# Kernel optimization log

Measured on AMD Instinct MI355X. Metric: run time of the kernel, lower is better.

## Reference

```python
import jax, jax.numpy as jnp
import numpy as np

N = 100000
E = 1600000
IN, HID, OUT = 128, 128, 64


def _sage_conv(x, edge_index, W_l, W_r, b):
    # PyG SAGEConv (aggr='mean'): out_i = W_l @ mean_{j->i} x_j + W_r @ x_i + b
    src, dst = edge_index[0], edge_index[1]
    msg = x[src]  # [E, d] gather
    agg = jax.ops.segment_sum(msg, dst, num_segments=N)  # [N, d]
    cnt = jax.ops.segment_sum(jnp.ones((edge_index.shape[1],), x.dtype), dst, num_segments=N)
    agg = agg / jnp.maximum(cnt, 1.0)[:, None]  # mean, safe for isolated nodes
    return agg @ W_l + x @ W_r + b


def setup_inputs() -> dict:
    key = jax.random.key(0)
    ks = jax.random.split(key, 8)
    x = jax.random.normal(ks[0], (N, IN), dtype=jnp.float32)
    W1_l = jax.random.normal(ks[1], (IN, HID), dtype=jnp.float32) / np.sqrt(IN)
    W1_r = jax.random.normal(ks[2], (IN, HID), dtype=jnp.float32) / np.sqrt(IN)
    b1 = jnp.zeros((HID,), dtype=jnp.float32)
    W2_l = jax.random.normal(ks[3], (HID, OUT), dtype=jnp.float32) / np.sqrt(HID)
    W2_r = jax.random.normal(ks[4], (HID, OUT), dtype=jnp.float32) / np.sqrt(HID)
    b2 = jnp.zeros((OUT,), dtype=jnp.float32)
    edge_index1 = jax.random.randint(ks[5], (2, E), 0, N, dtype=jnp.int64)
    edge_index2 = jax.random.randint(ks[6], (2, E), 0, N, dtype=jnp.int64)
    return {"x": x, "W1_l": W1_l, "W1_r": W1_r, "b1": b1,
            "W2_l": W2_l, "W2_r": W2_r, "b2": b2,
            "edge_index1": edge_index1, "edge_index2": edge_index2}


def reference(x, W1_l, W1_r, b1, W2_l, W2_r, b2, edge_index1, edge_index2):
    h = _sage_conv(x, edge_index1, W1_l, W1_r, b1)
    h = jax.nn.relu(h)
    h = _sage_conv(h, edge_index2, W2_l, W2_r, b2)
    return jax.nn.softmax(h, axis=1)
```

## Files before the change

kernel.cpp:

```cpp
#include <hip/hip_runtime.h>


#define FEAT 128
#define OUTF 64
#define BSH 9
#define BNODES 512
#define NBMAX 256
#define BUCKET_BLOCKS 512

typedef __attribute__((ext_vector_type(8))) short bf16x8;
typedef __attribute__((ext_vector_type(4))) float f32x4;

__device__ __forceinline__ unsigned f2bf_rne(float f) {
    unsigned u = __float_as_uint(f);
    return (u + 0x7fffu + ((u >> 16) & 1u)) >> 16;
}
__device__ __forceinline__ float bf_lo(unsigned u) { return __uint_as_float(u << 16); }
__device__ __forceinline__ float bf_hi(unsigned u) { return __uint_as_float(u & 0xffff0000u); }

__global__ void detect_idx_kernel(const unsigned* __restrict__ ei, unsigned* __restrict__ flag) {
    unsigned v = ei[2 * threadIdx.x + 1];
    if (v != 0u) atomicOr(flag, 1u);
}

__global__ __launch_bounds__(256) void convert_kernel(
    const float* __restrict__ in, unsigned short* __restrict__ outb, int total4) {
    for (int i = blockIdx.x * 256 + threadIdx.x; i < total4; i += gridDim.x * 256) {
        float4 v = *(const float4*)&in[(size_t)i * 4];
        ushort4 o;
        o.x = (unsigned short)f2bf_rne(v.x);
        o.y = (unsigned short)f2bf_rne(v.y);
        o.z = (unsigned short)f2bf_rne(v.z);
        o.w = (unsigned short)f2bf_rne(v.w);
        *(ushort4*)&outb[(size_t)i * 4] = o;
    }
}

__global__ __launch_bounds__(256) void init_cnt2_kernel(
    unsigned* __restrict__ cnt1, unsigned* __restrict__ cnt2, unsigned cap, int nb) {
    int i = blockIdx.x * 256 + threadIdx.x;
    if (i < nb) { cnt1[i] = (unsigned)i * cap; cnt2[i] = (unsigned)i * cap; }
}

__global__ __launch_bounds__(256) void bucket2_kernel(
    const void* __restrict__ ei1_raw, const void* __restrict__ ei2_raw,
    unsigned* __restrict__ pairs1, unsigned* __restrict__ pairs2,
    unsigned* __restrict__ cnt1, unsigned* __restrict__ cnt2,
    const unsigned* __restrict__ flag, int e1, int e2, unsigned cap, int nb) {
    __shared__ unsigned hist[NBMAX];
    __shared__ unsigned offs[NBMAX];
    const int tid = threadIdx.x;
    const bool is32 = (*flag != 0u);
    const int side = blockIdx.x / BUCKET_BLOCKS;
    const int bid = blockIdx.x % BUCKET_BLOCKS;
    const void* ei_raw = side ? ei2_raw : ei1_raw;
    unsigned* pairs = side ? pairs2 : pairs1;
    unsigned* cnt = side ? cnt2 : cnt1;
    const int nedge = side ? e2 : e1;
    const int chunk = (nedge + BUCKET_BLOCKS - 1) / BUCKET_BLOCKS;
    const int e0 = bid * chunk;
    const int eEnd = min(e0 + chunk, nedge);
    if (e0 >= nedge) return;

    for (int i = tid; i < nb; i += 256) hist[i] = 0u;
    __syncthreads();
    for (int e = e0 + tid; e < eEnd; e += 256) {
        int dst = is32 ? ((const int*)ei_raw)[nedge + e]
                       : (int)((const long long*)ei_raw)[nedge + e];
        atomicAdd(&hist[(unsigned)dst >> BSH], 1u);
    }
    __syncthreads();
    for (int i = tid; i < nb; i += 256) {
        unsigned c = hist[i];
        offs[i] = c ? atomicAdd(&cnt[i], c) : 0u;
    }
    __syncthreads();
    for (int e = e0 + tid; e < eEnd; e += 256) {
        int src, dst;
        if (is32) {
            const int* ei = (const int*)ei_raw;
            src = ei[e]; dst = ei[nedge + e];
        } else {
            const long long* ei = (const long long*)ei_raw;
            src = (int)ei[e]; dst = (int)ei[nedge + e];
        }
        unsigned b = (unsigned)dst >> BSH;
        unsigned pos = atomicAdd(&offs[b], 1u);
        if (pos < (b + 1u) * cap)
            pairs[pos] = (((unsigned)dst & (BNODES - 1u)) << 17) | (unsigned)src;
    }
}

__global__ __launch_bounds__(256) void csr2_kernel(
    const unsigned* __restrict__ pairs1, const unsigned* __restrict__ pairs2,
    const unsigned* __restrict__ cnt1, const unsigned* __restrict__ cnt2,
    unsigned* __restrict__ rps1, unsigned* __restrict__ rpe1,
    unsigned* __restrict__ rps2, unsigned* __restrict__ rpe2,
    int* __restrict__ esrc1, int* __restrict__ esrc2,
    unsigned cap, int n, int nb) {
    __shared__ unsigned hist[BNODES], excl[BNODES], offs[BNODES];
    __shared__ unsigned wsum[4], woff[4];
    const int side = blockIdx.x / nb;
    const int b = blockIdx.x % nb;
    const unsigned* pairs = side ? pairs2 : pairs1;
    const unsigned* cnt = side ? cnt2 : cnt1;
    unsigned* rps = side ? rps2 : rps1;
    unsigned* rpe = side ? rpe2 : rpe1;
    int* esrc = side ? esrc2 : esrc1;
    const int tid = threadIdx.x;
    const int lane = tid & 63;
    const unsigned base = (unsigned)b * cap;
    unsigned count = cnt[b] - base;
    if (count > cap) count = cap;

    hist[tid] = 0u; hist[tid + 256] = 0u;
    __syncthreads();
    for (unsigned e = tid; e < count; e += 256)
        atomicAdd(&hist[pairs[base + e] >> 17], 1u);
    __syncthreads();
    {
        unsigned s0 = hist[2 * tid], s1 = hist[2 * tid + 1];
        unsigned tsum = s0 + s1;
        unsigned incl = tsum;
        #pragma unroll
        for (int off = 1; off < 64; off <<= 1) {
            unsigned t = __shfl_up(incl, off, 64);
            if (lane >= off) incl += t;
        }
        if (lane == 63) wsum[tid >> 6] = incl;
        __syncthreads();
        if (tid == 0) {
            unsigned s = 0;
            #pragma unroll
            for (int w = 0; w < 4; ++w) { unsigned t = wsum[w]; woff[w] = s; s += t; }
        }
        __syncthreads();
        unsigned pre = woff[tid >> 6] + incl - tsum;
        excl[2 * tid] = pre;
        excl[2 * tid + 1] = pre + s0;
    }
    __syncthreads();
    #pragma unroll
    for (int h = 0; h < 2; ++h) {
        int lt = tid + h * 256;
        int node = b * BNODES + lt;
        if (node < n) {
            rps[node] = base + excl[lt];
            rpe[node] = base + excl[lt] + hist[lt];
        }
        offs[lt] = excl[lt];
    }
    __syncthreads();
    for (unsigned e = tid; e < count; e += 256) {
        unsigned p = pairs[base + e];
        unsigned lpos = atomicAdd(&offs[p >> 17], 1u);
        esrc[base + lpos] = (int)(p & 0x1FFFFu);
    }
}

#define ACC8(v)                                                              \
    a0 += bf_lo((v).x); a1 += bf_hi((v).x);                                  \
    a2 += bf_lo((v).y); a3 += bf_hi((v).y);                                  \
    a4 += bf_lo((v).z); a5 += bf_hi((v).z);                                  \
    a6 += bf_lo((v).w); a7 += bf_hi((v).w);

__global__ __launch_bounds__(256) void gather_mean128_kernel(
    const uint4* __restrict__ featq, const unsigned* __restrict__ rps,
    const unsigned* __restrict__ rpe, const int* __restrict__ esrc,
    uint4* __restrict__ aggq, int n) {
    const int wave = threadIdx.x >> 6;
    const int lane = threadIdx.x & 63;
    const int qi = lane >> 4;
    const int li = lane & 15;
    for (int node = blockIdx.x * 4 + wave; node < n; node += gridDim.x * 4) {
        unsigned rs = rps[node];
        unsigned re = rpe[node];
        float a0 = 0.f, a1 = 0.f, a2 = 0.f, a3 = 0.f;
        float a4 = 0.f, a5 = 0.f, a6 = 0.f, a7 = 0.f;
        unsigned j = rs;
        for (; j + 16 <= re; j += 16) {
            int i0 = esrc[j + qi];
            int i1 = esrc[j + 4 + qi];
            int i2 = esrc[j + 8 + qi];
            int i3 = esrc[j + 12 + qi];
            uint4 v0 = featq[(size_t)i0 * 16 + li];
            uint4 v1 = featq[(size_t)i1 * 16 + li];
            uint4 v2 = featq[(size_t)i2 * 16 + li];
            uint4 v3 = featq[(size_t)i3 * 16 + li];
            ACC8(v0); ACC8(v1); ACC8(v2); ACC8(v3);
        }
        for (; j + 8 <= re; j += 8) {
            int i0 = esrc[j + qi];
            int i1 = esrc[j + 4 + qi];
            uint4 v0 = featq[(size_t)i0 * 16 + li];
            uint4 v1 = featq[(size_t)i1 * 16 + li];
            ACC8(v0); ACC8(v1);
        }
        for (; j + 4 <= re; j += 4) {
            int i0 = esrc[j + qi];
            uint4 v0 = featq[(size_t)i0 * 16 + li];
            ACC8(v0);
        }
        unsigned rem = re - j;
        if ((unsigned)qi < rem) {
            int i0 = esrc[j + qi];
            uint4 v0 = featq[(size_t)i0 * 16 + li];
            ACC8(v0);
        }
        a0 += __shfl_xor(a0, 16, 64); a1 += __shfl_xor(a1, 16, 64);
        a2 += __shfl_xor(a2, 16, 64); a3 += __shfl_xor(a3, 16, 64);
        a4 += __shfl_xor(a4, 16, 64); a5 += __shfl_xor(a5, 16, 64);
        a6 += __shfl_xor(a6, 16, 64); a7 += __shfl_xor(a7, 16, 64);
        a0 += __shfl_xor(a0, 32, 64); a1 += __shfl_xor(a1, 32, 64);
        a2 += __shfl_xor(a2, 32, 64); a3 += __shfl_xor(a3, 32, 64);
        a4 += __shfl_xor(a4, 32, 64); a5 += __shfl_xor(a5, 32, 64);
        a6 += __shfl_xor(a6, 32, 64); a7 += __shfl_xor(a7, 32, 64);
        if (lane < 16) {
            float inv = (re > rs) ? 1.0f / (float)(re - rs) : 0.0f;
            uint4 o;
            o.x = f2bf_rne(a0 * inv) | (f2bf_rne(a1 * inv) << 16);
            o.y = f2bf_rne(a2 * inv) | (f2bf_rne(a3 * inv) << 16);
            o.z = f2bf_rne(a4 * inv) | (f2bf_rne(a5 * inv) << 16);
            o.w = f2bf_rne(a6 * inv) | (f2bf_rne(a7 * inv) << 16);
            aggq[(size_t)node * 16 + lane] = o;
        }
    }
}

__global__ __launch_bounds__(256) void gather_mean64_kernel(
    const uint4* __restrict__ y2q, const unsigned* __restrict__ rps,
    const unsigned* __restrict__ rpe, const int* __restrict__ esrc,
    uint4* __restrict__ aggyq, int n) {
    const int wave = threadIdx.x >> 6;
    const int lane = threadIdx.x & 63;
    const int oi = lane >> 3;
    const int li = lane & 7;
    for (int node = blockIdx.x * 4 + wave; node < n; node += gridDim.x * 4) {
        unsigned rs = rps[node];
        unsigned re = rpe[node];
        float a0 = 0.f, a1 = 0.f, a2 = 0.f, a3 = 0.f;
        float a4 = 0.f, a5 = 0.f, a6 = 0.f, a7 = 0.f;
        unsigned j = rs;
        for (; j + 16 <= re; j += 16) {
            int i0 = esrc[j + oi];
            int i1 = esrc[j + 8 + oi];
            uint4 v0 = y2q[(size_t)i0 * 8 + li];
            uint4 v1 = y2q[(size_t)i1 * 8 + li];
            ACC8(v0); ACC8(v1);
        }
        for (; j + 8 <= re; j += 8) {
            int i0 = esrc[j + oi];
            uint4 v0 = y2q[(size_t)i0 * 8 + li];
            ACC8(v0);
        }
        unsigned rem = re - j;
        if ((unsigned)oi < rem) {
            int i0 = esrc[j + oi];
            uint4 v0 = y2q[(size_t)i0 * 8 + li];
            ACC8(v0);
        }
        a0 += __shfl_xor(a0, 8, 64);  a1 += __shfl_xor(a1, 8, 64);
        a2 += __shfl_xor(a2, 8, 64);  a3 += __shfl_xor(a3, 8, 64);
        a4 += __shfl_xor(a4, 8, 64);  a5 += __shfl_xor(a5, 8, 64);
        a6 += __shfl_xor(a6, 8, 64);  a7 += __shfl_xor(a7, 8, 64);
        a0 += __shfl_xor(a0, 16, 64); a1 += __shfl_xor(a1, 16, 64);
        a2 += __shfl_xor(a2, 16, 64); a3 += __shfl_xor(a3, 16, 64);
        a4 += __shfl_xor(a4, 16, 64); a5 += __shfl_xor(a5, 16, 64);
        a6 += __shfl_xor(a6, 16, 64); a7 += __shfl_xor(a7, 16, 64);
        a0 += __shfl_xor(a0, 32, 64); a1 += __shfl_xor(a1, 32, 64);
        a2 += __shfl_xor(a2, 32, 64); a3 += __shfl_xor(a3, 32, 64);
        a4 += __shfl_xor(a4, 32, 64); a5 += __shfl_xor(a5, 32, 64);
        a6 += __shfl_xor(a6, 32, 64); a7 += __shfl_xor(a7, 32, 64);
        if (lane < 8) {
            float inv = (re > rs) ? 1.0f / (float)(re - rs) : 0.0f;
            uint4 o;
            o.x = f2bf_rne(a0 * inv) | (f2bf_rne(a1 * inv) << 16);
            o.y = f2bf_rne(a2 * inv) | (f2bf_rne(a3 * inv) << 16);
            o.z = f2bf_rne(a4 * inv) | (f2bf_rne(a5 * inv) << 16);
            o.w = f2bf_rne(a6 * inv) | (f2bf_rne(a7 * inv) << 16);
            aggyq[(size_t)node * 8 + lane] = o;
        }
    }
}

__global__ __launch_bounds__(256, 2) void gemm1_kernel(
    const unsigned short* __restrict__ agg, const unsigned short* __restrict__ xb,
    const float* __restrict__ Wl, const float* __restrict__ Wr,
    const float* __restrict__ b, unsigned short* __restrict__ hb, int n) {
    __shared__ __align__(16) unsigned short sB[256 * FEAT];
    const int tid = threadIdx.x;

    for (int idx = tid; idx < 256 * FEAT; idx += 256) {
        int k = idx >> 7, col = idx & 127;
        float w = (k < 128) ? Wl[k * FEAT + col] : Wr[(k - 128) * FEAT + col];
        int pos = ((col >> 4) * 8 + (k >> 5)) * 512
                + ((((k >> 3) & 3) * 16 + (col & 15)) * 8) + (k & 7);
        sB[pos] = (unsigned short)f2bf_rne(w);
    }
    __syncthreads();

    const int wv = tid >> 6, lane = tid & 63;
    const int cg = wv & 1;
    const int ms = wv >> 1;
    const int g = lane >> 4, c15 = lane & 15;

    bf16x8 bf[4][8];
    #pragma unroll
    for (int ct = 0; ct < 4; ++ct)
        #pragma unroll
        for (int ks = 0; ks < 8; ++ks)
            bf[ct][ks] = *(const bf16x8*)&sB[(((cg * 4 + ct) * 8 + ks) * 64 + lane) * 8];

    float bias[4];
    #pragma unroll
    for (int ct = 0; ct < 4; ++ct) bias[ct] = b[cg * 64 + ct * 16 + c15];

    const int ntiles = (n + 31) >> 5;
    for (int tile = blockIdx.x; tile < ntiles; tile += gridDim.x) {
        const int base = tile * 32;
        const int row = base + ms * 16 + c15;
        bf16x8 af[8];
        #pragma unroll
        for (int ks = 0; ks < 8; ++ks) {
            bf16x8 a = {0, 0, 0, 0, 0, 0, 0, 0};
            if (row < n) {
                int karr = ks * 32 + g * 8;
                const unsigned short* p = (ks < 4)
                    ? &agg[(size_t)row * FEAT + karr]
                    : &xb[(size_t)row * FEAT + (karr - 128)];
                a = *(const bf16x8*)p;
            }
            af[ks] = a;
        }
        f32x4 z = {0.f, 0.f, 0.f, 0.f};
        f32x4 acc[4] = {z, z, z, z};
        #pragma unroll
        for (int ks = 0; ks < 8; ++ks)
            #pragma unroll
            for (int ct = 0; ct < 4; ++ct)
                acc[ct] = __builtin_amdgcn_mfma_f32_16x16x32_bf16(
                    af[ks], bf[ct][ks], acc[ct], 0, 0, 0);
        #pragma unroll
        for (int ct = 0; ct < 4; ++ct) {
            const int col = cg * 64 + ct * 16 + c15;
            #pragma unroll
            for (int r = 0; r < 4; ++r) {
                int node = base + ms * 16 + g * 4 + r;
                if (node < n) {
                    float v = fmaxf(acc[ct][r] + bias[ct], 0.f);
                    hb[(size_t)node * FEAT + col] = (unsigned short)f2bf_rne(v);
                }
            }
        }
    }
}

__global__ __launch_bounds__(256, 2) void gemmy2_kernel(
    const unsigned short* __restrict__ hb, const float* __restrict__ Wl,
    unsigned short* __restrict__ y2, int n) {
    __shared__ __align__(16) unsigned short sB[128 * OUTF];
    const int tid = threadIdx.x;

    for (int idx = tid; idx < 128 * OUTF; idx += 256) {
        int k = idx >> 6, col = idx & 63;
        float w = Wl[k * OUTF + col];
        int pos = ((col >> 4) * 4 + (k >> 5)) * 512
                + ((((k >> 3) & 3) * 16 + (col & 15)) * 8) + (k & 7);
        sB[pos] = (unsigned short)f2bf_rne(w);
    }
    __syncthreads();

    const int wv = tid >> 6, lane = tid & 63;
    const int g = lane >> 4, c15 = lane & 15;

    bf16x8 bf[4][4];
    #pragma unroll
    for (int ct = 0; ct < 4; ++ct)
        #pragma unroll
        for (int ks = 0; ks < 4; ++ks)
            bf[ct][ks] = *(const bf16x8*)&sB[((ct * 4 + ks) * 64 + lane) * 8];

    const int ntiles = (n + 63) >> 6;
    for (int tile = blockIdx.x; tile < ntiles; tile += gridDim.x) {
        const int base = tile * 64;
        const int row = base + wv * 16 + c15;
        bf16x8 af[4];
        #pragma unroll
        for (int ks = 0; ks < 4; ++ks) {
            bf16x8 a = {0, 0, 0, 0, 0, 0, 0, 0};
            if (row < n) a = *(const bf16x8*)&hb[(size_t)row * FEAT + ks * 32 + g * 8];
            af[ks] = a;
        }
        f32x4 z = {0.f, 0.f, 0.f, 0.f};
        f32x4 acc[4] = {z, z, z, z};
        #pragma unroll
        for (int ks = 0; ks < 4; ++ks)
            #pragma unroll
            for (int ct = 0; ct < 4; ++ct)
                acc[ct] = __builtin_amdgcn_mfma_f32_16x16x32_bf16(
                    af[ks], bf[ct][ks], acc[ct], 0, 0, 0);
        #pragma unroll
        for (int ct = 0; ct < 4; ++ct) {
            const int col = ct * 16 + c15;
            #pragma unroll
            for (int r = 0; r < 4; ++r) {
                int node = base + wv * 16 + g * 4 + r;
                if (node < n)
                    y2[(size_t)node * OUTF + col] = (unsigned short)f2bf_rne(acc[ct][r]);
            }
        }
    }
}

__global__ __launch_bounds__(256, 2) void gemm2b_kernel(
    const unsigned short* __restrict__ hb, const unsigned short* __restrict__ aggy,
    const float* __restrict__ Wr, const float* __restrict__ b,
    float* __restrict__ out, int n) {
    __shared__ __align__(16) unsigned short sB[128 * OUTF];
    const int tid = threadIdx.x;

    for (int idx = tid; idx < 128 * OUTF; idx += 256) {
        int k = idx >> 6, col = idx & 63;
        float w = Wr[k * OUTF + col];
        int pos = ((col >> 4) * 4 + (k >> 5)) * 512
                + ((((k >> 3) & 3) * 16 + (col & 15)) * 8) + (k & 7);
        sB[pos] = (unsigned short)f2bf_rne(w);
    }
    __syncthreads();

    const int wv = tid >> 6, lane = tid & 63;
    const int g = lane >> 4, c15 = lane & 15;

    bf16x8 bf[4][4];
    #pragma unroll
    for (int ct = 0; ct < 4; ++ct)
        #pragma unroll
        for (int ks = 0; ks < 4; ++ks)
            bf[ct][ks] = *(const bf16x8*)&sB[((ct * 4 + ks) * 64 + lane) * 8];

    float bias[4];
    #pragma unroll
    for (int ct = 0; ct < 4; ++ct) bias[ct] = b[ct * 16 + c15];

    const int ntiles = (n + 63) >> 6;
    for (int tile = blockIdx.x; tile < ntiles; tile += gridDim.x) {
        const int base = tile * 64;
        const int row = base + wv * 16 + c15;
        bf16x8 af[4];
        #pragma unroll
        for (int ks = 0; ks < 4; ++ks) {
            bf16x8 a = {0, 0, 0, 0, 0, 0, 0, 0};
            if (row < n) a = *(const bf16x8*)&hb[(size_t)row * FEAT + ks * 32 + g * 8];
            af[ks] = a;
        }
        f32x4 z = {0.f, 0.f, 0.f, 0.f};
        f32x4 acc[4] = {z, z, z, z};
        #pragma unroll
        for (int ks = 0; ks < 4; ++ks)
            #pragma unroll
            for (int ct = 0; ct < 4; ++ct)
                acc[ct] = __builtin_amdgcn_mfma_f32_16x16x32_bf16(
                    af[ks], bf[ct][ks], acc[ct], 0, 0, 0);

        #pragma unroll
        for (int r = 0; r < 4; ++r) {
            int node = base + wv * 16 + g * 4 + r;
            bool ok = node < n;
            float v[4];
            #pragma unroll
            for (int ct = 0; ct < 4; ++ct) {
                float my = 0.f;
                if (ok) {
                    unsigned short u = aggy[(size_t)node * OUTF + ct * 16 + c15];
                    my = __uint_as_float((unsigned)u << 16);
                }
                v[ct] = acc[ct][r] + bias[ct] + my;
            }
            float m = fmaxf(fmaxf(v[0], v[1]), fmaxf(v[2], v[3]));
            #pragma unroll
            for (int off = 8; off > 0; off >>= 1)
                m = fmaxf(m, __shfl_xor(m, off, 64));
            float e0 = __expf(v[0] - m), e1 = __expf(v[1] - m);
            float e2 = __expf(v[2] - m), e3 = __expf(v[3] - m);
            float s = e0 + e1 + e2 + e3;
            #pragma unroll
            for (int off = 8; off > 0; off >>= 1)
                s += __shfl_xor(s, off, 64);
            float inv = 1.0f / s;
            if (ok) {
                out[(size_t)node * OUTF + c15]      = e0 * inv;
                out[(size_t)node * OUTF + 16 + c15] = e1 * inv;
                out[(size_t)node * OUTF + 32 + c15] = e2 * inv;
                out[(size_t)node * OUTF + 48 + c15] = e3 * inv;
            }
        }
    }
}

extern "C" void kernel_launch(void* const* d_in, const int* in_sizes, int n_in,
                              void* d_out, int out_size, void* d_ws, size_t ws_size,
                              hipStream_t stream) {
    const float* x   = (const float*)d_in[0];
    const float* W1l = (const float*)d_in[1];
    const float* W1r = (const float*)d_in[2];
    const float* b1  = (const float*)d_in[3];
    const float* W2l = (const float*)d_in[4];
    const float* W2r = (const float*)d_in[5];
    const float* b2  = (const float*)d_in[6];
    const void*  ei1 = d_in[7];
    const void*  ei2 = d_in[8];
    float* out = (float*)d_out;

    const int n  = in_sizes[0] / FEAT;
    const int e1 = in_sizes[7] / 2;
    const int e2 = in_sizes[8] / 2;
    const int emax = (e1 > e2) ? e1 : e2;

    const int nb = (n + BNODES - 1) >> BSH;
    if (nb > NBMAX) return;
    unsigned cap = (unsigned)(emax / nb + emax / (4 * nb) + 512);
    cap = (cap + 63u) & ~63u;

    char* ws = (char*)d_ws;
    const size_t fBytes   = (size_t)n * FEAT * 2;
    const size_t cntBytes = ((size_t)NBMAX * 4 + 255) & ~(size_t)255;
    const size_t rpBytes  = (((size_t)n * 4) + 255) & ~(size_t)255;
    const size_t bktBytes = (((size_t)nb * cap * 4) + 255) & ~(size_t)255;
    if (2 * bktBytes > fBytes) return;
    unsigned*       flag = (unsigned*)ws;
    unsigned short* xb   = (unsigned short*)(ws + 256);
    unsigned short* hb   = (unsigned short*)(ws + 256 + fBytes);
    char*           aggr = ws + 256 + 2 * fBytes;
    unsigned short* agg  = (unsigned short*)aggr;
    unsigned short* y2   = agg;
    unsigned short* aggy = agg + (size_t)n * OUTF;
    unsigned* pairs1 = (unsigned*)aggr;
    unsigned* pairs2 = (unsigned*)(aggr + bktBytes);
    char* p = ws + 256 + 3 * fBytes;
    unsigned* cnt1 = (unsigned*)p;            p += cntBytes;
    unsigned* cnt2 = (unsigned*)p;            p += cntBytes;
    unsigned* rps1 = (unsigned*)p;            p += rpBytes;
    unsigned* rpe1 = (unsigned*)p;            p += rpBytes;
    unsigned* rps2 = (unsigned*)p;            p += rpBytes;
    unsigned* rpe2 = (unsigned*)p;            p += rpBytes;
    int*      esrc1 = (int*)p;                p += bktBytes;
    int*      esrc2 = (int*)p;                p += bktBytes;
    p += 256;
    if ((size_t)(p - ws) > ws_size) return;

    hipMemsetAsync(flag, 0, 4, stream);
    detect_idx_kernel<<<1, 256, 0, stream>>>((const unsigned*)ei1, flag);
    convert_kernel<<<2048, 256, 0, stream>>>(x, xb, in_sizes[0] / 4);

    const int gatherGrid = (n + 3) / 4;

    init_cnt2_kernel<<<(nb + 255) / 256, 256, 0, stream>>>(cnt1, cnt2, cap, nb);
    bucket2_kernel<<<2 * BUCKET_BLOCKS, 256, 0, stream>>>(
        ei1, ei2, pairs1, pairs2, cnt1, cnt2, flag, e1, e2, cap, nb);
    csr2_kernel<<<2 * nb, 256, 0, stream>>>(
        pairs1, pairs2, cnt1, cnt2, rps1, rpe1, rps2, rpe2, esrc1, esrc2, cap, n, nb);

    gather_mean128_kernel<<<gatherGrid, 256, 0, stream>>>((const uint4*)xb, rps1, rpe1,
                                                          esrc1, (uint4*)agg, n);
    gemm1_kernel<<<640, 256, 0, stream>>>(agg, xb, W1l, W1r, b1, hb, n);

    gemmy2_kernel<<<512, 256, 0, stream>>>(hb, W2l, y2, n);
    gather_mean64_kernel<<<gatherGrid, 256, 0, stream>>>((const uint4*)y2, rps2, rpe2,
                                                         esrc2, (uint4*)aggy, n);
    gemm2b_kernel<<<512, 256, 0, stream>>>(hb, aggy, W2r, b2, out, n);
}
```

Baseline: 265.5 us.

## Stage bucket scatter through shared-memory local sort for coalesced writes

The edge bucketing kernel now processes its edge chunk in stages of 2048 edges. Each stage builds a local histogram, sorts the packed pairs by bucket in shared memory, and then writes them to global memory in runs that are contiguous per bucket. This replaces the random per-edge scatter with more coalesced stores. In exchange it adds a serial single-thread prefix scan per stage, extra barriers, and more shared-memory use, which may lower occupancy.

```diff
diff --git a/kernel.cpp b/kernel.cpp
--- a/kernel.cpp
+++ b/kernel.cpp
@@ -7,6 +7,7 @@
 #define BNODES 512
 #define NBMAX 256
 #define BUCKET_BLOCKS 512
+#define STAGE 2048
 
 typedef __attribute__((ext_vector_type(8))) short bf16x8;
 typedef __attribute__((ext_vector_type(4))) float f32x4;
@@ -48,7 +49,12 @@
     unsigned* __restrict__ cnt1, unsigned* __restrict__ cnt2,
     const unsigned* __restrict__ flag, int e1, int e2, unsigned cap, int nb) {
     __shared__ unsigned hist[NBMAX];
-    __shared__ unsigned offs[NBMAX];
+    __shared__ unsigned wcur[NBMAX];
+    __shared__ unsigned lhist[NBMAX];
+    __shared__ unsigned lseg[NBMAX];
+    __shared__ unsigned loffs[NBMAX];
+    __shared__ unsigned sorted[STAGE];
+    __shared__ unsigned char sbid[STAGE];
     const int tid = threadIdx.x;
     const bool is32 = (*flag != 0u);
     const int side = blockIdx.x / BUCKET_BLOCKS;
@@ -72,22 +78,55 @@
     __syncthreads();
     for (int i = tid; i < nb; i += 256) {
         unsigned c = hist[i];
-        offs[i] = c ? atomicAdd(&cnt[i], c) : 0u;
-    }
-    __syncthreads();
-    for (int e = e0 + tid; e < eEnd; e += 256) {
-        int src, dst;
-        if (is32) {
-            const int* ei = (const int*)ei_raw;
-            src = ei[e]; dst = ei[nedge + e];
-        } else {
-            const long long* ei = (const long long*)ei_raw;
-            src = (int)ei[e]; dst = (int)ei[nedge + e];
-        }
-        unsigned b = (unsigned)dst >> BSH;
-        unsigned pos = atomicAdd(&offs[b], 1u);
-        if (pos < (b + 1u) * cap)
-            pairs[pos] = (((unsigned)dst & (BNODES - 1u)) << 17) | (unsigned)src;
+        wcur[i] = c ? atomicAdd(&cnt[i], c) : 0u;
+    }
+    __syncthreads();
+
+    for (int s0 = e0; s0 < eEnd; s0 += STAGE) {
+        const int sEnd = min(s0 + STAGE, eEnd);
+        const int cs = sEnd - s0;
+        for (int i = tid; i < nb; i += 256) lhist[i] = 0u;
+        __syncthreads();
+        unsigned myp[STAGE / 256];
+        unsigned char myb[STAGE / 256];
+        int mycnt = 0;
+        for (int e = s0 + tid; e < sEnd; e += 256) {
+            int src, dst;
+            if (is32) {
+                const int* ei = (const int*)ei_raw;
+                src = ei[e]; dst = ei[nedge + e];
+            } else {
+                const long long* ei = (const long long*)ei_raw;
+                src = (int)ei[e]; dst = (int)ei[nedge + e];
+            }
+            unsigned b = (unsigned)dst >> BSH;
+            myp[mycnt] = (((unsigned)dst & (BNODES - 1u)) << 17) | (unsigned)src;
+            myb[mycnt] = (unsigned char)b;
+            ++mycnt;
+            atomicAdd(&lhist[b], 1u);
+        }
+        __syncthreads();
+        if (tid == 0) {
+            unsigned s = 0;
+            for (int i = 0; i < nb; ++i) { lseg[i] = s; loffs[i] = s; s += lhist[i]; }
+        }
+        __syncthreads();
+        for (int k = 0; k < mycnt; ++k) {
+            unsigned b = myb[k];
+            unsigned p = atomicAdd(&loffs[b], 1u);
+            sorted[p] = myp[k];
+            sbid[p] = (unsigned char)b;
+        }
+        __syncthreads();
+        for (int i = tid; i < cs; i += 256) {
+            unsigned b = sbid[i];
+            unsigned pos = wcur[b] + ((unsigned)i - lseg[b]);
+            if (pos < (b + 1u) * cap)
+                pairs[pos] = sorted[i];
+        }
+        __syncthreads();
+        for (int i = tid; i < nb; i += 256) wcur[i] += lhist[i];
+        __syncthreads();
     }
 }
 
```

Result: no change. 263.8 us (-0.6%).
